# Kernel tuning notes

Hardware: AMD Instinct MI355X
Metric: run time of the kernel (lower is better)

## Reference

```python
import jax, jax.numpy as jnp
import numpy as np

B, S, I, H = 64, 1024, 512, 512


def setup_inputs() -> dict:
    key = jax.random.key(0)
    ks = jax.random.split(key, 20)
    s = (1.0 / H) ** 0.5
    u = lambda k, shape: jax.random.uniform(k, shape, jnp.float32, -s, s)
    inp = {
        "inputs": jax.random.normal(ks[0], (B, S, I), jnp.float32),
        "h0": jnp.zeros((B, H), jnp.float32),
        "c0": jnp.zeros((B, H), jnp.float32),
        "w_ii": u(ks[1], (H, I)), "w_if": u(ks[2], (H, I)),
        "w_ig": u(ks[3], (H, I)), "w_io": u(ks[4], (H, I)),
        "w_hi": u(ks[5], (H, H)), "w_hf": u(ks[6], (H, H)),
        "w_hg": u(ks[7], (H, H)), "w_ho": u(ks[8], (H, H)),
        "b_ii": u(ks[9], (H,)), "b_if": u(ks[10], (H,)),
        "b_ig": u(ks[11], (H,)), "b_io": u(ks[12], (H,)),
        "b_hi": u(ks[13], (H,)), "b_hf": u(ks[14], (H,)),
        "b_ho": u(ks[15], (H,)), "b_hg": u(ks[16], (H,)),
    }
    return inp


def reference(inputs, h0, c0, w_ii, w_if, w_ig, w_io, w_hi, w_hf, w_hg, w_ho,
              b_ii, b_if, b_ig, b_io, b_hi, b_hf, b_hg, b_ho):
    hidden = w_hi.shape[0]
    # Stack the 4 input-to-hidden gates -> one (4H, I) matrix; same math as 4 matmuls.
    Wi = jnp.concatenate([w_ii, w_if, w_ig, w_io], axis=0)          # (4H, I)
    Wh = jnp.concatenate([w_hi, w_hf, w_hg, w_ho], axis=0)          # (4H, H)
    b = (jnp.concatenate([b_ii, b_if, b_ig, b_io])
         + jnp.concatenate([b_hi, b_hf, b_hg, b_ho]))               # (4H,)
    # Precompute all input projections: (B, S, 4H) -> scan only does recurrent part.
    x_proj = jnp.einsum('bsi,gi->bsg', inputs, Wi) + b

    def step(carry, x_t):
        h, c = carry
        gates = x_t + h @ Wh.T                                      # (B, 4H)
        i_t = jax.nn.sigmoid(gates[:, 0 * hidden:1 * hidden])
        f_t = jax.nn.sigmoid(gates[:, 1 * hidden:2 * hidden])
        g_t = jnp.tanh(gates[:, 2 * hidden:3 * hidden])
        o_t = jax.nn.sigmoid(gates[:, 3 * hidden:4 * hidden])
        c = f_t * c + i_t * g_t
        h = o_t * jnp.tanh(c)
        return (h, c), h

    (h_f, c_f), outs = jax.lax.scan(step, (h0, c0),
                                    jnp.swapaxes(x_proj, 0, 1))     # outs: (S, B, H)
    output_final = jnp.swapaxes(outs, 0, 1)                         # (B, S, H)
    return output_final, (h_f, c_f)
```

## Files before the change

### kernel.cpp

```cpp
#include <hip/hip_runtime.h>

typedef unsigned short u16;
typedef unsigned long long u64;
typedef __attribute__((ext_vector_type(8))) short short8;
typedef __attribute__((ext_vector_type(4))) float f4;
typedef __attribute__((ext_vector_type(4))) unsigned short us4;

#define MFMA_BF16(a, b, c) __builtin_amdgcn_mfma_f32_16x16x32_bf16((a), (b), (c), 0, 0, 0)

#define Bsz 64
#define Ssz 1024
#define Isz 512
#define Hsz 512
#define G4  2048
#define SCH 128
#define NCHUNK 8
#define SCAN_NB 64

#define WS_FLAG  0
#define WS_BIAS  262144
#define WS_HBUF  270336
#define WS_CBUF  401408
#define WS_WI    532480
#define WS_WH    2629632
#define WS_XC    4726784

#define HF_OFF ((size_t)Bsz * Ssz * Hsz)
#define CF_OFF (HF_OFF + (size_t)Bsz * Hsz)

__device__ __forceinline__ u16 bf16rne(float f) {
    unsigned int x = __float_as_uint(f);
    unsigned int r = (x + 0x7fffu + ((x >> 16) & 1u)) >> 16;
    return (u16)r;
}
__device__ __forceinline__ float sigf(float x) { return 1.0f / (1.0f + __expf(-x)); }
__device__ __forceinline__ float tanh_(float x) { return 1.0f - 2.0f / (__expf(2.0f * x) + 1.0f); }

struct PrepArgs {
    const float* h0; const float* c0;
    const float* wi[4]; const float* wh[4];
    const float* bi[4]; const float* bh[4];
    u16* Wi; u16* Wh; float* bias; u16* hbuf; float* cbuf; int* flag;
};
#define PREP_TOT (1048576 + 1048576 + 2048 + 32768 + 32768 + 65536)

__global__ void lstm_prep(PrepArgs a) {
    long i = (long)blockIdx.x * 256 + threadIdx.x;
    if (i < 1048576) {
        int rowp = (int)(i >> 9), k = (int)(i & 511);
        int unit = rowp >> 2, gate = rowp & 3;
        a.Wi[i] = bf16rne(a.wi[gate][unit * Isz + k]);
    } else if (i < 2097152) {
        long j = i - 1048576;
        int rowp = (int)(j >> 9), k = (int)(j & 511);
        int unit = rowp >> 2, gate = rowp & 3;
        a.Wh[j] = bf16rne(a.wh[gate][unit * Hsz + k]);
    } else if (i < 2097152 + 2048) {
        int j = (int)(i - 2097152);
        int unit = j >> 2, gate = j & 3;
        a.bias[j] = a.bi[gate][unit] + a.bh[gate][unit];
    } else if (i < 2097152 + 2048 + 32768) {
        int j = (int)(i - (2097152 + 2048));
        __hip_atomic_store(&a.hbuf[32768 + j], bf16rne(a.h0[j]),
                           __ATOMIC_RELAXED, __HIP_MEMORY_SCOPE_AGENT);
    } else if (i < 2097152 + 2048 + 65536) {
        int j = (int)(i - (2097152 + 2048 + 32768));
        a.cbuf[j] = a.c0[j];
    } else if (i < PREP_TOT) {
        __hip_atomic_store(&a.flag[i - (2097152 + 2048 + 65536)], 0,
                           __ATOMIC_RELAXED, __HIP_MEMORY_SCOPE_AGENT);
    }
}

__global__ __launch_bounds__(256) void xproj_gemm(
    const float* __restrict__ inp, const u16* __restrict__ Wi,
    float* __restrict__ xc, int t0)
{
    __shared__ u16 Al[128 * 40];
    __shared__ u16 Bl[128 * 40];
    const int tid = threadIdx.x;
    const int L = tid & 63, w = tid >> 6;
    const int q = L >> 4, lm = L & 15;
    const int nt = blockIdx.x & 15, b = blockIdx.x >> 4;
    const float* Abase = inp + ((size_t)b * Ssz + t0) * Isz;
    const u16* Bbase = Wi + (size_t)nt * 128 * Isz;
    const int mh = (w & 1) * 64, nh = (w >> 1) * 64;

    f4 acc[4][4];
#pragma unroll
    for (int i = 0; i < 4; ++i)
#pragma unroll
        for (int j = 0; j < 4; ++j) acc[i][j] = (f4){0.f, 0.f, 0.f, 0.f};

    for (int kt = 0; kt < 16; ++kt) {
        const int k0 = kt * 32;
#pragma unroll
        for (int r = 0; r < 4; ++r) {
            int flat = tid + r * 256;
            int m = flat >> 3, kq = flat & 7;
            f4 v = *(const f4*)(Abase + (size_t)m * Isz + k0 + kq * 4);
            us4 h = {bf16rne(v.x), bf16rne(v.y), bf16rne(v.z), bf16rne(v.w)};
            *(us4*)(&Al[m * 40 + kq * 4]) = h;
        }
#pragma unroll
        for (int r = 0; r < 2; ++r) {
            int flat = tid + r * 256;
            int n = flat >> 2, kq = flat & 3;
            *(short8*)(&Bl[n * 40 + kq * 8]) =
                *(const short8*)(Bbase + (size_t)n * Isz + k0 + kq * 8);
        }
        __syncthreads();
        short8 af[4], bfr[4];
#pragma unroll
        for (int i = 0; i < 4; ++i)
            af[i] = *(const short8*)(&Al[(mh + i * 16 + lm) * 40 + q * 8]);
#pragma unroll
        for (int j = 0; j < 4; ++j)
            bfr[j] = *(const short8*)(&Bl[(nh + j * 16 + lm) * 40 + q * 8]);
#pragma unroll
        for (int i = 0; i < 4; ++i)
#pragma unroll
            for (int j = 0; j < 4; ++j)
                acc[i][j] = MFMA_BF16(af[i], bfr[j], acc[i][j]);
        __syncthreads();
    }
    float* Obase = xc + (size_t)b * SCH * G4 + (size_t)nt * 128;
#pragma unroll
    for (int i = 0; i < 4; ++i)
#pragma unroll
        for (int j = 0; j < 4; ++j)
#pragma unroll
            for (int r = 0; r < 4; ++r) {
                int m = mh + i * 16 + q * 4 + r;
                int n = nh + j * 16 + lm;
                Obase[(size_t)m * G4 + n] = acc[i][j][r];
            }
}

__global__ __launch_bounds__(256, 1) void lstm_scan(
    const float* __restrict__ xc, const u16* __restrict__ Whp,
    const float* __restrict__ bias, u16* __restrict__ hbuf,
    float* __restrict__ cbuf, int* __restrict__ flag,
    float* __restrict__ out, int t0)
{
    __shared__ float gate_buf[64 * 32];
    const int tid = threadIdx.x, bid = blockIdx.x;
    const int L = tid & 63, w = tid >> 6;
    const int q = L >> 4, lm = L & 15;
    const int row0 = bid * 32;
    const int j0 = bid * 8;
    const int myb = w * 16 + lm;

    short8 wb[16][2];
#pragma unroll
    for (int kt = 0; kt < 16; ++kt)
#pragma unroll
        for (int jt = 0; jt < 2; ++jt) {
            int n = row0 + jt * 16 + lm;
            wb[kt][jt] = *(const short8*)(Whp + (size_t)n * Hsz + kt * 32 + q * 8);
        }

    const int be = tid >> 2;
    const int u0 = (tid & 3) * 2;
    const f4 bias0 = *(const f4*)(bias + row0 + u0 * 4);
    const f4 bias1 = *(const f4*)(bias + row0 + u0 * 4 + 4);
    float c0r = cbuf[be * Hsz + j0 + u0];
    float c1r = cbuf[be * Hsz + j0 + u0 + 1];

    for (int t = t0; t < t0 + SCH; ++t) {
        const int sl = t - t0;
        const float* xrow = xc + ((size_t)be * SCH + sl) * G4 + row0 + u0 * 4;
        f4 xv0 = *(const f4*)(xrow);
        f4 xv1 = *(const f4*)(xrow + 4);

        if (t > t0) {
            if (w == 0) {
                const int* fl = flag + (t - 1) * 64;
                int v;
                do {
                    v = __hip_atomic_load(&fl[L], __ATOMIC_RELAXED,
                                          __HIP_MEMORY_SCOPE_AGENT);
                } while (!__all(v));
            }
            __syncthreads();
            __asm__ volatile("" ::: "memory");
        }

        const u64* hq = (const u64*)(hbuf + (size_t)((t & 1) ^ 1) * 32768)
                        + (size_t)myb * 128;
        union { short8 v; u64 q2[2]; } au[16];
#pragma unroll
        for (int kt = 0; kt < 16; ++kt) {
            au[kt].q2[0] = __hip_atomic_load(hq + kt * 8 + q * 2,
                                             __ATOMIC_RELAXED, __HIP_MEMORY_SCOPE_AGENT);
            au[kt].q2[1] = __hip_atomic_load(hq + kt * 8 + q * 2 + 1,
                                             __ATOMIC_RELAXED, __HIP_MEMORY_SCOPE_AGENT);
        }

        f4 acc0 = (f4){0.f, 0.f, 0.f, 0.f}, acc1 = acc0;
#pragma unroll
        for (int kt = 0; kt < 16; ++kt) {
            acc0 = MFMA_BF16(au[kt].v, wb[kt][0], acc0);
            acc1 = MFMA_BF16(au[kt].v, wb[kt][1], acc1);
        }

#pragma unroll
        for (int r = 0; r < 4; ++r) {
            int brow = w * 16 + q * 4 + r;
            gate_buf[brow * 32 + lm] = acc0[r];
            gate_buf[brow * 32 + 16 + lm] = acc1[r];
        }
        __syncthreads();

        f4 g0 = *(const f4*)(&gate_buf[be * 32 + u0 * 4]);
        f4 g1 = *(const f4*)(&gate_buf[be * 32 + u0 * 4 + 4]);
        g0 += xv0 + bias0;
        g1 += xv1 + bias1;
        float i1 = sigf(g0.x), f1 = sigf(g0.y), gg1 = tanh_(g0.z), o1 = sigf(g0.w);
        c0r = f1 * c0r + i1 * gg1;
        float h1 = o1 * tanh_(c0r);
        float i2 = sigf(g1.x), f2 = sigf(g1.y), gg2 = tanh_(g1.z), o2 = sigf(g1.w);
        c1r = f2 * c1r + i2 * gg2;
        float h2 = o2 * tanh_(c1r);

        unsigned int hv = (unsigned int)bf16rne(h1) | ((unsigned int)bf16rne(h2) << 16);
        unsigned int* hw = (unsigned int*)(hbuf + (size_t)(t & 1) * 32768
                                           + be * Hsz + j0 + u0);
        __hip_atomic_store(hw, hv, __ATOMIC_RELAXED, __HIP_MEMORY_SCOPE_AGENT);

        float* op = out + ((size_t)be * Ssz + t) * Hsz + j0 + u0;
        op[0] = h1;
        op[1] = h2;
        if (t == Ssz - 1) {
            out[HF_OFF + be * Hsz + j0 + u0] = h1;
            out[HF_OFF + be * Hsz + j0 + u0 + 1] = h2;
            out[CF_OFF + be * Hsz + j0 + u0] = c0r;
            out[CF_OFF + be * Hsz + j0 + u0 + 1] = c1r;
        }

        __syncthreads();
        if (tid == 0) {
            __asm__ volatile("" ::: "memory");
            __hip_atomic_store(&flag[t * 64 + bid], 1,
                               __ATOMIC_RELAXED, __HIP_MEMORY_SCOPE_AGENT);
        }
    }
    cbuf[be * Hsz + j0 + u0] = c0r;
    cbuf[be * Hsz + j0 + u0 + 1] = c1r;
}

extern "C" void kernel_launch(void* const* d_in, const int* in_sizes, int n_in,
                              void* d_out, int out_size, void* d_ws, size_t ws_size,
                              hipStream_t stream) {
    const float* inputs = (const float*)d_in[0];
    char* W = (char*)d_ws;
    int*  flag = (int*)(W + WS_FLAG);
    float* bias = (float*)(W + WS_BIAS);
    u16*  hbuf = (u16*)(W + WS_HBUF);
    float* cbuf = (float*)(W + WS_CBUF);
    u16*  Wi   = (u16*)(W + WS_WI);
    u16*  Wh   = (u16*)(W + WS_WH);
    float* xch  = (float*)(W + WS_XC);

    PrepArgs a;
    a.h0 = (const float*)d_in[1];
    a.c0 = (const float*)d_in[2];
    for (int g = 0; g < 4; ++g) {
        a.wi[g] = (const float*)d_in[3 + g];
        a.wh[g] = (const float*)d_in[7 + g];
        a.bi[g] = (const float*)d_in[11 + g];
    }
    a.bh[0] = (const float*)d_in[15];
    a.bh[1] = (const float*)d_in[16];
    a.bh[2] = (const float*)d_in[18];
    a.bh[3] = (const float*)d_in[17];
    a.Wi = Wi; a.Wh = Wh; a.bias = bias; a.hbuf = hbuf; a.cbuf = cbuf; a.flag = flag;

    lstm_prep<<<(PREP_TOT + 255) / 256, 256, 0, stream>>>(a);

    float* out = (float*)d_out;
    for (int c = 0; c < NCHUNK; ++c) {
        int t0 = c * SCH;
        xproj_gemm<<<dim3(64 * 16), 256, 0, stream>>>(inputs, Wi, xch, t0);
        lstm_scan<<<dim3(SCAN_NB), 256, 0, stream>>>(xch, Wh, bias, hbuf, cbuf, flag, out, t0);
    }
}
```

Measured before the change: 7.562 ms.

## Replace per-step flag barrier with epoch-tagged hidden-state values in scan

Each stored bf16 hidden value now carries a 16-bit step tag in its upper half. Readers spin directly on the h buffer until every tag matches the expected step, instead of waiting on a separate per-block flag array followed by a block barrier. This removes the flag write, one __syncthreads per step and the separate flag poll, and the gate buffer is double-buffered in LDS so the trailing barrier can go. A per-launch epoch counter keeps tags distinct across calls, at the cost of doubling the h buffer's size and read traffic and making every h read a spin loop.

```diff
diff --git a/kernel.cpp b/kernel.cpp
--- a/kernel.cpp
+++ b/kernel.cpp
@@ -1,6 +1,7 @@
 #include <hip/hip_runtime.h>
 
 typedef unsigned short u16;
+typedef unsigned int u32;
 typedef unsigned long long u64;
 typedef __attribute__((ext_vector_type(8))) short short8;
 typedef __attribute__((ext_vector_type(4))) float f4;
@@ -17,13 +18,13 @@
 #define NCHUNK 8
 #define SCAN_NB 64
 
-#define WS_FLAG  0
-#define WS_BIAS  262144
-#define WS_HBUF  270336
-#define WS_CBUF  401408
-#define WS_WI    532480
-#define WS_WH    2629632
-#define WS_XC    4726784
+#define WS_EPOCH 0
+#define WS_BIAS  4096
+#define WS_HBUF  16384
+#define WS_CBUF  278528
+#define WS_WI    409600
+#define WS_WH    2506752
+#define WS_XC    4603904
 
 #define HF_OFF ((size_t)Bsz * Ssz * Hsz)
 #define CF_OFF (HF_OFF + (size_t)Bsz * Hsz)
@@ -36,13 +37,18 @@
 __device__ __forceinline__ float sigf(float x) { return 1.0f / (1.0f + __expf(-x)); }
 __device__ __forceinline__ float tanh_(float x) { return 1.0f - 2.0f / (__expf(2.0f * x) + 1.0f); }
 
+__global__ void epoch_bump(u32* e) {
+    u32 v = __hip_atomic_load(e, __ATOMIC_RELAXED, __HIP_MEMORY_SCOPE_AGENT);
+    __hip_atomic_store(e, v + 1u, __ATOMIC_RELAXED, __HIP_MEMORY_SCOPE_AGENT);
+}
+
 struct PrepArgs {
     const float* h0; const float* c0;
     const float* wi[4]; const float* wh[4];
     const float* bi[4]; const float* bh[4];
-    u16* Wi; u16* Wh; float* bias; u16* hbuf; float* cbuf; int* flag;
+    u16* Wi; u16* Wh; float* bias; u32* hbuf; float* cbuf; const u32* epoch;
 };
-#define PREP_TOT (1048576 + 1048576 + 2048 + 32768 + 32768 + 65536)
+#define PREP_TOT (1048576 + 1048576 + 2048 + 32768 + 32768)
 
 __global__ void lstm_prep(PrepArgs a) {
     long i = (long)blockIdx.x * 256 + threadIdx.x;
@@ -61,14 +67,13 @@
         a.bias[j] = a.bi[gate][unit] + a.bh[gate][unit];
     } else if (i < 2097152 + 2048 + 32768) {
         int j = (int)(i - (2097152 + 2048));
-        __hip_atomic_store(&a.hbuf[32768 + j], bf16rne(a.h0[j]),
+        u32 ep = __hip_atomic_load(a.epoch, __ATOMIC_RELAXED, __HIP_MEMORY_SCOPE_AGENT);
+        u32 tg = ((ep * 2048u - 1u) & 0xffffu) << 16;
+        __hip_atomic_store(&a.hbuf[32768 + j], tg | (u32)bf16rne(a.h0[j]),
                            __ATOMIC_RELAXED, __HIP_MEMORY_SCOPE_AGENT);
-    } else if (i < 2097152 + 2048 + 65536) {
+    } else if (i < PREP_TOT) {
         int j = (int)(i - (2097152 + 2048 + 32768));
         a.cbuf[j] = a.c0[j];
-    } else if (i < PREP_TOT) {
-        __hip_atomic_store(&a.flag[i - (2097152 + 2048 + 65536)], 0,
-                           __ATOMIC_RELAXED, __HIP_MEMORY_SCOPE_AGENT);
     }
 }
 
@@ -139,11 +144,11 @@
 
 __global__ __launch_bounds__(256, 1) void lstm_scan(
     const float* __restrict__ xc, const u16* __restrict__ Whp,
-    const float* __restrict__ bias, u16* __restrict__ hbuf,
-    float* __restrict__ cbuf, int* __restrict__ flag,
+    const float* __restrict__ bias, u32* __restrict__ hbuf,
+    float* __restrict__ cbuf, const u32* __restrict__ epoch_p,
     float* __restrict__ out, int t0)
 {
-    __shared__ float gate_buf[64 * 32];
+    __shared__ float gate_buf[2][64 * 32];
     const int tid = threadIdx.x, bid = blockIdx.x;
     const int L = tid & 63, w = tid >> 6;
     const int q = L >> 4, lm = L & 15;
@@ -151,6 +156,9 @@
     const int j0 = bid * 8;
     const int myb = w * 16 + lm;
 
+    const u32 ebase = __hip_atomic_load(epoch_p, __ATOMIC_RELAXED,
+                                        __HIP_MEMORY_SCOPE_AGENT) * 2048u;
+
     short8 wb[16][2];
 #pragma unroll
     for (int kt = 0; kt < 16; ++kt)
@@ -173,28 +181,26 @@
         f4 xv0 = *(const f4*)(xrow);
         f4 xv1 = *(const f4*)(xrow + 4);
 
-        if (t > t0) {
-            if (w == 0) {
-                const int* fl = flag + (t - 1) * 64;
-                int v;
-                do {
-                    v = __hip_atomic_load(&fl[L], __ATOMIC_RELAXED,
-                                          __HIP_MEMORY_SCOPE_AGENT);
-                } while (!__all(v));
-            }
-            __syncthreads();
-            __asm__ volatile("" ::: "memory");
-        }
-
+        const u32 texp = ((ebase + (u32)(t - 1)) & 0xffffu) << 16;
         const u64* hq = (const u64*)(hbuf + (size_t)((t & 1) ^ 1) * 32768)
-                        + (size_t)myb * 128;
-        union { short8 v; u64 q2[2]; } au[16];
-#pragma unroll
-        for (int kt = 0; kt < 16; ++kt) {
-            au[kt].q2[0] = __hip_atomic_load(hq + kt * 8 + q * 2,
-                                             __ATOMIC_RELAXED, __HIP_MEMORY_SCOPE_AGENT);
-            au[kt].q2[1] = __hip_atomic_load(hq + kt * 8 + q * 2 + 1,
-                                             __ATOMIC_RELAXED, __HIP_MEMORY_SCOPE_AGENT);
+                        + (size_t)myb * 256;
+        union AU { u32 u[4]; short8 v; } au[16];
+        for (;;) {
+            u32 bad = 0;
+#pragma unroll
+            for (int kt = 0; kt < 16; ++kt)
+#pragma unroll
+                for (int m = 0; m < 4; ++m) {
+                    u64 r = __hip_atomic_load(hq + kt * 16 + q * 4 + m,
+                                              __ATOMIC_RELAXED,
+                                              __HIP_MEMORY_SCOPE_AGENT);
+                    u32 lo = (u32)r;
+                    u32 hi = (u32)(r >> 32);
+                    bad |= ((lo ^ texp) | (hi ^ texp)) & 0xffff0000u;
+                    au[kt].u[m] = (lo & 0xffffu) | (hi << 16);
+                }
+            if (__all(bad == 0)) break;
+            __builtin_amdgcn_s_sleep(1);
         }
 
         f4 acc0 = (f4){0.f, 0.f, 0.f, 0.f}, acc1 = acc0;
@@ -204,28 +210,30 @@
             acc1 = MFMA_BF16(au[kt].v, wb[kt][1], acc1);
         }
 
+        float* gb = gate_buf[t & 1];
 #pragma unroll
         for (int r = 0; r < 4; ++r) {
             int brow = w * 16 + q * 4 + r;
-            gate_buf[brow * 32 + lm] = acc0[r];
-            gate_buf[brow * 32 + 16 + lm] = acc1[r];
+            gb[brow * 32 + lm] = acc0[r];
+            gb[brow * 32 + 16 + lm] = acc1[r];
         }
         __syncthreads();
 
-        f4 g0 = *(const f4*)(&gate_buf[be * 32 + u0 * 4]);
-        f4 g1 = *(const f4*)(&gate_buf[be * 32 + u0 * 4 + 4]);
+        f4 g0 = *(const f4*)(&gb[be * 32 + u0 * 4]);
+        f4 g1 = *(const f4*)(&gb[be * 32 + u0 * 4 + 4]);
         g0 += xv0 + bias0;
         g1 += xv1 + bias1;
         float i1 = sigf(g0.x), f1 = sigf(g0.y), gg1 = tanh_(g0.z), o1 = sigf(g0.w);
         c0r = f1 * c0r + i1 * gg1;
         float h1 = o1 * tanh_(c0r);
-        float i2 = sigf(g1.x), f2 = sigf(g1.y), gg2 = tanh_(g1.z), o2 = sigf(g1.w);
-        c1r = f2 * c1r + i2 * gg2;
+        float i2 = sigf(g1.x), fg2 = sigf(g1.y), gg2 = tanh_(g1.z), o2 = sigf(g1.w);
+        c1r = fg2 * c1r + i2 * gg2;
         float h2 = o2 * tanh_(c1r);
 
-        unsigned int hv = (unsigned int)bf16rne(h1) | ((unsigned int)bf16rne(h2) << 16);
-        unsigned int* hw = (unsigned int*)(hbuf + (size_t)(t & 1) * 32768
-                                           + be * Hsz + j0 + u0);
+        u32 tg = ((ebase + (u32)t) & 0xffffu) << 16;
+        u64 hv = (u64)(tg | (u32)bf16rne(h1))
+               | ((u64)(tg | (u32)bf16rne(h2)) << 32);
+        u64* hw = (u64*)(hbuf + (size_t)(t & 1) * 32768 + be * Hsz + j0 + u0);
         __hip_atomic_store(hw, hv, __ATOMIC_RELAXED, __HIP_MEMORY_SCOPE_AGENT);
 
         float* op = out + ((size_t)be * Ssz + t) * Hsz + j0 + u0;
@@ -237,13 +245,6 @@
             out[CF_OFF + be * Hsz + j0 + u0] = c0r;
             out[CF_OFF + be * Hsz + j0 + u0 + 1] = c1r;
         }
-
-        __syncthreads();
-        if (tid == 0) {
-            __asm__ volatile("" ::: "memory");
-            __hip_atomic_store(&flag[t * 64 + bid], 1,
-                               __ATOMIC_RELAXED, __HIP_MEMORY_SCOPE_AGENT);
-        }
     }
     cbuf[be * Hsz + j0 + u0] = c0r;
     cbuf[be * Hsz + j0 + u0 + 1] = c1r;
@@ -254,9 +255,9 @@
                               hipStream_t stream) {
     const float* inputs = (const float*)d_in[0];
     char* W = (char*)d_ws;
-    int*  flag = (int*)(W + WS_FLAG);
+    u32*  epoch = (u32*)(W + WS_EPOCH);
     float* bias = (float*)(W + WS_BIAS);
-    u16*  hbuf = (u16*)(W + WS_HBUF);
+    u32*  hbuf = (u32*)(W + WS_HBUF);
     float* cbuf = (float*)(W + WS_CBUF);
     u16*  Wi   = (u16*)(W + WS_WI);
     u16*  Wh   = (u16*)(W + WS_WH);
@@ -274,14 +275,15 @@
     a.bh[1] = (const float*)d_in[16];
     a.bh[2] = (const float*)d_in[18];
     a.bh[3] = (const float*)d_in[17];
-    a.Wi = Wi; a.Wh = Wh; a.bias = bias; a.hbuf = hbuf; a.cbuf = cbuf; a.flag = flag;
-
+    a.Wi = Wi; a.Wh = Wh; a.bias = bias; a.hbuf = hbuf; a.cbuf = cbuf; a.epoch = epoch;
+
+    epoch_bump<<<1, 1, 0, stream>>>(epoch);
     lstm_prep<<<(PREP_TOT + 255) / 256, 256, 0, stream>>>(a);
 
     float* out = (float*)d_out;
     for (int c = 0; c < NCHUNK; ++c) {
         int t0 = c * SCH;
         xproj_gemm<<<dim3(64 * 16), 256, 0, stream>>>(inputs, Wi, xch, t0);
-        lstm_scan<<<dim3(SCAN_NB), 256, 0, stream>>>(xch, Wh, bias, hbuf, cbuf, flag, out, t0);
-    }
-}
+        lstm_scan<<<dim3(SCAN_NB), 256, 0, stream>>>(xch, Wh, bias, hbuf, cbuf, epoch, out, t0);
+    }
+}
```

After: 13.36 ms. 76.7% more time.

## Use per-wave flags in LSTM scan and drop block barriers per step

Applied to the files above, without the earlier changes.

Each wave now publishes its own per-step flag and waits only on the flags of the matching wave slice across all blocks. This removes the two block-wide __syncthreads per timestep and the single-wave poll followed by a barrier, and adds s_sleep backoff to the spin. The recurrent weights move from registers to LDS, which frees registers at the cost of LDS reads every step. Correctness now depends on each wave's gate_buf rows and h slice being independent; the flag region and workspace offsets grow to match.

```diff
diff --git a/kernel.cpp b/kernel.cpp
--- a/kernel.cpp
+++ b/kernel.cpp
@@ -1,6 +1,7 @@
 #include <hip/hip_runtime.h>
 
 typedef unsigned short u16;
+typedef unsigned int u32;
 typedef unsigned long long u64;
 typedef __attribute__((ext_vector_type(8))) short short8;
 typedef __attribute__((ext_vector_type(4))) float f4;
@@ -18,12 +19,12 @@
 #define SCAN_NB 64
 
 #define WS_FLAG  0
-#define WS_BIAS  262144
-#define WS_HBUF  270336
-#define WS_CBUF  401408
-#define WS_WI    532480
-#define WS_WH    2629632
-#define WS_XC    4726784
+#define WS_BIAS  1048576
+#define WS_HBUF  1056768
+#define WS_CBUF  1187840
+#define WS_WI    1318912
+#define WS_WH    3416064
+#define WS_XC    5513216
 
 #define HF_OFF ((size_t)Bsz * Ssz * Hsz)
 #define CF_OFF (HF_OFF + (size_t)Bsz * Hsz)
@@ -42,7 +43,7 @@
     const float* bi[4]; const float* bh[4];
     u16* Wi; u16* Wh; float* bias; u16* hbuf; float* cbuf; int* flag;
 };
-#define PREP_TOT (1048576 + 1048576 + 2048 + 32768 + 32768 + 65536)
+#define PREP_TOT (1048576 + 1048576 + 2048 + 32768 + 32768 + 262144)
 
 __global__ void lstm_prep(PrepArgs a) {
     long i = (long)blockIdx.x * 256 + threadIdx.x;
@@ -61,14 +62,12 @@
         a.bias[j] = a.bi[gate][unit] + a.bh[gate][unit];
     } else if (i < 2097152 + 2048 + 32768) {
         int j = (int)(i - (2097152 + 2048));
-        __hip_atomic_store(&a.hbuf[32768 + j], bf16rne(a.h0[j]),
-                           __ATOMIC_RELAXED, __HIP_MEMORY_SCOPE_AGENT);
+        a.hbuf[32768 + j] = bf16rne(a.h0[j]);
     } else if (i < 2097152 + 2048 + 65536) {
         int j = (int)(i - (2097152 + 2048 + 32768));
         a.cbuf[j] = a.c0[j];
     } else if (i < PREP_TOT) {
-        __hip_atomic_store(&a.flag[i - (2097152 + 2048 + 65536)], 0,
-                           __ATOMIC_RELAXED, __HIP_MEMORY_SCOPE_AGENT);
+        a.flag[i - (2097152 + 2048 + 65536)] = 0;
     }
 }
 
@@ -143,7 +142,8 @@
     float* __restrict__ cbuf, int* __restrict__ flag,
     float* __restrict__ out, int t0)
 {
-    __shared__ float gate_buf[64 * 32];
+    __shared__ u16 whl[16384];
+    __shared__ float gb[64 * 36];
     const int tid = threadIdx.x, bid = blockIdx.x;
     const int L = tid & 63, w = tid >> 6;
     const int q = L >> 4, lm = L & 15;
@@ -151,14 +151,14 @@
     const int j0 = bid * 8;
     const int myb = w * 16 + lm;
 
-    short8 wb[16][2];
-#pragma unroll
-    for (int kt = 0; kt < 16; ++kt)
-#pragma unroll
-        for (int jt = 0; jt < 2; ++jt) {
-            int n = row0 + jt * 16 + lm;
-            wb[kt][jt] = *(const short8*)(Whp + (size_t)n * Hsz + kt * 32 + q * 8);
-        }
+#pragma unroll
+    for (int i = 0; i < 8; ++i) {
+        int f = tid + i * 256;
+        int qq = f & 3, lmm = (f >> 2) & 15, ktt = (f >> 6) & 15, jtt = f >> 10;
+        *(short8*)(&whl[f * 8]) =
+            *(const short8*)(Whp + (size_t)(row0 + jtt * 16 + lmm) * Hsz
+                             + ktt * 32 + qq * 8);
+    }
 
     const int be = tid >> 2;
     const int u0 = (tid & 3) * 2;
@@ -167,23 +167,23 @@
     float c0r = cbuf[be * Hsz + j0 + u0];
     float c1r = cbuf[be * Hsz + j0 + u0 + 1];
 
+    __syncthreads();
+
     for (int t = t0; t < t0 + SCH; ++t) {
         const int sl = t - t0;
         const float* xrow = xc + ((size_t)be * SCH + sl) * G4 + row0 + u0 * 4;
         f4 xv0 = *(const f4*)(xrow);
         f4 xv1 = *(const f4*)(xrow + 4);
 
-        if (t > t0) {
-            if (w == 0) {
-                const int* fl = flag + (t - 1) * 64;
-                int v;
-                do {
-                    v = __hip_atomic_load(&fl[L], __ATOMIC_RELAXED,
-                                          __HIP_MEMORY_SCOPE_AGENT);
-                } while (!__all(v));
-            }
-            __syncthreads();
-            __asm__ volatile("" ::: "memory");
+        if (t > 0) {
+            const int* fl = flag + (size_t)(t - 1) * 256 + w * 64;
+            int v;
+            do {
+                v = __hip_atomic_load(&fl[L], __ATOMIC_RELAXED,
+                                      __HIP_MEMORY_SCOPE_AGENT);
+                if (__all(v)) break;
+                __builtin_amdgcn_s_sleep(1);
+            } while (1);
         }
 
         const u64* hq = (const u64*)(hbuf + (size_t)((t & 1) ^ 1) * 32768)
@@ -200,33 +200,37 @@
         f4 acc0 = (f4){0.f, 0.f, 0.f, 0.f}, acc1 = acc0;
 #pragma unroll
         for (int kt = 0; kt < 16; ++kt) {
-            acc0 = MFMA_BF16(au[kt].v, wb[kt][0], acc0);
-            acc1 = MFMA_BF16(au[kt].v, wb[kt][1], acc1);
+            short8 b0 = *(const short8*)(&whl[kt * 512 + lm * 32 + q * 8]);
+            short8 b1 = *(const short8*)(&whl[(16 + kt) * 512 + lm * 32 + q * 8]);
+            acc0 = MFMA_BF16(au[kt].v, b0, acc0);
+            acc1 = MFMA_BF16(au[kt].v, b1, acc1);
         }
 
 #pragma unroll
         for (int r = 0; r < 4; ++r) {
             int brow = w * 16 + q * 4 + r;
-            gate_buf[brow * 32 + lm] = acc0[r];
-            gate_buf[brow * 32 + 16 + lm] = acc1[r];
-        }
-        __syncthreads();
-
-        f4 g0 = *(const f4*)(&gate_buf[be * 32 + u0 * 4]);
-        f4 g1 = *(const f4*)(&gate_buf[be * 32 + u0 * 4 + 4]);
+            gb[brow * 36 + lm] = acc0[r];
+            gb[brow * 36 + 16 + lm] = acc1[r];
+        }
+        f4 g0 = *(const f4*)(&gb[be * 36 + u0 * 4]);
+        f4 g1 = *(const f4*)(&gb[be * 36 + u0 * 4 + 4]);
+
         g0 += xv0 + bias0;
         g1 += xv1 + bias1;
         float i1 = sigf(g0.x), f1 = sigf(g0.y), gg1 = tanh_(g0.z), o1 = sigf(g0.w);
         c0r = f1 * c0r + i1 * gg1;
         float h1 = o1 * tanh_(c0r);
-        float i2 = sigf(g1.x), f2 = sigf(g1.y), gg2 = tanh_(g1.z), o2 = sigf(g1.w);
-        c1r = f2 * c1r + i2 * gg2;
+        float i2 = sigf(g1.x), fg2 = sigf(g1.y), gg2 = tanh_(g1.z), o2 = sigf(g1.w);
+        c1r = fg2 * c1r + i2 * gg2;
         float h2 = o2 * tanh_(c1r);
 
-        unsigned int hv = (unsigned int)bf16rne(h1) | ((unsigned int)bf16rne(h2) << 16);
-        unsigned int* hw = (unsigned int*)(hbuf + (size_t)(t & 1) * 32768
-                                           + be * Hsz + j0 + u0);
+        u32 hv = (u32)bf16rne(h1) | ((u32)bf16rne(h2) << 16);
+        u32* hw = (u32*)(hbuf + (size_t)(t & 1) * 32768 + be * Hsz + j0 + u0);
         __hip_atomic_store(hw, hv, __ATOMIC_RELAXED, __HIP_MEMORY_SCOPE_AGENT);
+        asm volatile("s_waitcnt vmcnt(0)" ::: "memory");
+        if (L == 0)
+            __hip_atomic_store(&flag[(size_t)t * 256 + w * 64 + bid], 1,
+                               __ATOMIC_RELAXED, __HIP_MEMORY_SCOPE_AGENT);
 
         float* op = out + ((size_t)be * Ssz + t) * Hsz + j0 + u0;
         op[0] = h1;
@@ -236,13 +240,6 @@
             out[HF_OFF + be * Hsz + j0 + u0 + 1] = h2;
             out[CF_OFF + be * Hsz + j0 + u0] = c0r;
             out[CF_OFF + be * Hsz + j0 + u0 + 1] = c1r;
-        }
-
-        __syncthreads();
-        if (tid == 0) {
-            __asm__ volatile("" ::: "memory");
-            __hip_atomic_store(&flag[t * 64 + bid], 1,
-                               __ATOMIC_RELAXED, __HIP_MEMORY_SCOPE_AGENT);
         }
     }
     cbuf[be * Hsz + j0 + u0] = c0r;
```

Measured after the change: 7.942 ms. 1.05x slower.
